# Performance work log

Hardware: AMD Instinct MI355X
Metric: run time of the kernel (lower is better)

Reference implementation:

```python
import jax, jax.numpy as jnp
import numpy as np

GAMMA = 1.0

C, K, D = 10000, 4, 2048  # classes, prototypes per class, feature dim


def setup_inputs() -> dict:
    key = jax.random.key(0)
    k1, k2 = jax.random.split(key)
    feature = jax.random.normal(k1, (D,), dtype=jnp.float32)
    all_prototypes = jax.random.normal(k2, (C, K, D), dtype=jnp.float32)
    label = 7
    return {"feature": feature, "label": label, "all_prototypes": all_prototypes}


def reference(feature, label, all_prototypes):
    # squared euclidean distance from feature to every prototype: [C, K]
    diff = all_prototypes - feature  # broadcast [C,K,D]
    d = jnp.sum(diff * diff, axis=-1)  # [C,K]
    logits = -GAMMA * d  # [C,K]
    # denominator: one = sum_{c,k} exp(-gamma * d_{c,k}); use stable logsumexp
    log_one = jax.nn.logsumexp(logits)
    # probability = sum_k -log(exp(logits[label,k]) / one)
    #             = sum_k (gamma * d[label,k] + log(one))
    lbl_logits = jax.lax.dynamic_index_in_dim(logits, label, axis=0, keepdims=False)  # [K]
    probability = jnp.sum(log_one - lbl_logits)
    return probability
```

## Files before the change

kernel.cpp:

```cpp
#include <hip/hip_runtime.h>

#define C_CLASSES 10000
#define K_PROTO   4
#define D_DIM     2048
#define ROWS      (C_CLASSES * K_PROTO)
#define D_VEC     (D_DIM / 4)

__global__ __launch_bounds__(256) void dist_kernel(const float4* __restrict__ proto,
                                                   const float4* __restrict__ feat,
                                                   float* __restrict__ d_row) {
    const int wave = threadIdx.x >> 6;
    const int lane = threadIdx.x & 63;
    const int row  = blockIdx.x * 4 + wave;
    const float4* p = proto + (size_t)row * D_VEC;

    float acc = 0.0f;
#pragma unroll
    for (int j = 0; j < 8; ++j) {
        const int idx = j * 64 + lane;
        const float4 pv = p[idx];
        const float4 fv = feat[idx];
        const float dx = pv.x - fv.x;
        const float dy = pv.y - fv.y;
        const float dz = pv.z - fv.z;
        const float dw = pv.w - fv.w;
        acc += dx * dx + dy * dy + dz * dz + dw * dw;
    }
#pragma unroll
    for (int off = 32; off > 0; off >>= 1)
        acc += __shfl_down(acc, off, 64);
    if (lane == 0) d_row[row] = acc;
}

__global__ __launch_bounds__(256) void finalize_kernel(const float* __restrict__ d_row,
                                                       const int* __restrict__ label,
                                                       float* __restrict__ out) {
    __shared__ float red[256];
    const int tid = threadIdx.x;

    float lmin = 3.402823466e38f;
    for (int i = tid; i < ROWS; i += 256)
        lmin = fminf(lmin, d_row[i]);
    red[tid] = lmin;
    __syncthreads();
    for (int s = 128; s > 0; s >>= 1) {
        if (tid < s) red[tid] = fminf(red[tid], red[tid + s]);
        __syncthreads();
    }
    const float dmin = red[0];
    __syncthreads();

    float lsum = 0.0f;
    for (int i = tid; i < ROWS; i += 256)
        lsum += expf(dmin - d_row[i]);
    red[tid] = lsum;
    __syncthreads();
    for (int s = 128; s > 0; s >>= 1) {
        if (tid < s) red[tid] += red[tid + s];
        __syncthreads();
    }

    if (tid == 0) {
        const float log_one = -dmin + logf(red[0]);
        const int lbl = label[0];
        float p = 0.0f;
#pragma unroll
        for (int k = 0; k < K_PROTO; ++k)
            p += log_one + d_row[lbl * K_PROTO + k];
        out[0] = p;
    }
}

extern "C" void kernel_launch(void* const* d_in, const int* in_sizes, int n_in,
                              void* d_out, int out_size, void* d_ws, size_t ws_size,
                              hipStream_t stream) {
    const float* feat  = (const float*)d_in[0];
    const int*   label = (const int*)d_in[1];
    const float* proto = (const float*)d_in[2];
    float* out   = (float*)d_out;
    float* d_row = (float*)d_ws;

    dist_kernel<<<ROWS / 4, 256, 0, stream>>>(
        (const float4*)proto, (const float4*)feat, d_row);
    finalize_kernel<<<1, 256, 0, stream>>>(d_row, label, out);
}
```

Before: 476.2 us.

## Process five rows per wave and fuse partial logsumexp into distance kernel

```diff
diff --git a/kernel.cpp b/kernel.cpp
--- a/kernel.cpp
+++ b/kernel.cpp
@@ -5,43 +5,73 @@
 #define D_DIM     2048
 #define ROWS      (C_CLASSES * K_PROTO)
 #define D_VEC     (D_DIM / 4)
+#define RPW       5
+#define NBLOCKS   2000
+#define NWAVES    (NBLOCKS * 4)
 
 __global__ __launch_bounds__(256) void dist_kernel(const float4* __restrict__ proto,
                                                    const float4* __restrict__ feat,
-                                                   float* __restrict__ d_row) {
-    const int wave = threadIdx.x >> 6;
+                                                   const int* __restrict__ label,
+                                                   float* __restrict__ wave_min,
+                                                   float* __restrict__ wave_sum,
+                                                   float* __restrict__ d_label) {
+    const int wave = (blockIdx.x << 2) | (threadIdx.x >> 6);
     const int lane = threadIdx.x & 63;
-    const int row  = blockIdx.x * 4 + wave;
-    const float4* p = proto + (size_t)row * D_VEC;
+    const int row0 = wave * RPW;
+    const int lbl  = label[0];
 
-    float acc = 0.0f;
+    float4 f[8];
 #pragma unroll
-    for (int j = 0; j < 8; ++j) {
-        const int idx = j * 64 + lane;
-        const float4 pv = p[idx];
-        const float4 fv = feat[idx];
-        const float dx = pv.x - fv.x;
-        const float dy = pv.y - fv.y;
-        const float dz = pv.z - fv.z;
-        const float dw = pv.w - fv.w;
-        acc += dx * dx + dy * dy + dz * dz + dw * dw;
+    for (int j = 0; j < 8; ++j) f[j] = feat[j * 64 + lane];
+
+    float d[RPW];
+#pragma unroll
+    for (int r = 0; r < RPW; ++r) {
+        const float4* p = proto + (size_t)(row0 + r) * D_VEC;
+        float acc = 0.0f;
+#pragma unroll
+        for (int j = 0; j < 8; ++j) {
+            const float4 pv = p[j * 64 + lane];
+            const float dx = pv.x - f[j].x;
+            const float dy = pv.y - f[j].y;
+            const float dz = pv.z - f[j].z;
+            const float dw = pv.w - f[j].w;
+            acc += dx * dx + dy * dy + dz * dz + dw * dw;
+        }
+#pragma unroll
+        for (int mask = 1; mask < 64; mask <<= 1)
+            acc += __shfl_xor(acc, mask, 64);
+        d[r] = acc;
     }
+
+    float mw = d[0];
 #pragma unroll
-    for (int off = 32; off > 0; off >>= 1)
-        acc += __shfl_down(acc, off, 64);
-    if (lane == 0) d_row[row] = acc;
+    for (int r = 1; r < RPW; ++r) mw = fminf(mw, d[r]);
+    float sw = 0.0f;
+#pragma unroll
+    for (int r = 0; r < RPW; ++r) sw += expf(mw - d[r]);
+
+    if (lane == 0) {
+        wave_min[wave] = mw;
+        wave_sum[wave] = sw;
+#pragma unroll
+        for (int r = 0; r < RPW; ++r) {
+            const int row = row0 + r;
+            if ((row >> 2) == lbl) d_label[row & 3] = d[r];
+        }
+    }
 }
 
-__global__ __launch_bounds__(256) void finalize_kernel(const float* __restrict__ d_row,
-                                                       const int* __restrict__ label,
+__global__ __launch_bounds__(256) void finalize_kernel(const float* __restrict__ wave_min,
+                                                       const float* __restrict__ wave_sum,
+                                                       const float* __restrict__ d_label,
                                                        float* __restrict__ out) {
     __shared__ float red[256];
     const int tid = threadIdx.x;
 
-    float lmin = 3.402823466e38f;
-    for (int i = tid; i < ROWS; i += 256)
-        lmin = fminf(lmin, d_row[i]);
-    red[tid] = lmin;
+    float m = 3.402823466e38f;
+    for (int i = tid; i < NWAVES; i += 256) m = fminf(m, wave_min[i]);
+    red[tid] = m;
     __syncthreads();
     for (int s = 128; s > 0; s >>= 1) {
         if (tid < s) red[tid] = fminf(red[tid], red[tid + s]);
@@ -50,10 +80,10 @@
     const float dmin = red[0];
     __syncthreads();
 
-    float lsum = 0.0f;
-    for (int i = tid; i < ROWS; i += 256)
-        lsum += expf(dmin - d_row[i]);
-    red[tid] = lsum;
+    float acc = 0.0f;
+    for (int i = tid; i < NWAVES; i += 256)
+        acc += wave_sum[i] * expf(dmin - wave_min[i]);
+    red[tid] = acc;
     __syncthreads();
     for (int s = 128; s > 0; s >>= 1) {
         if (tid < s) red[tid] += red[tid + s];
@@ -62,11 +92,9 @@
 
     if (tid == 0) {
         const float log_one = -dmin + logf(red[0]);
-        const int lbl = label[0];
         float p = 0.0f;
 #pragma unroll
-        for (int k = 0; k < K_PROTO; ++k)
-            p += log_one + d_row[lbl * K_PROTO + k];
+        for (int k = 0; k < K_PROTO; ++k) p += log_one + d_label[k];
         out[0] = p;
     }
 }
@@ -77,10 +105,14 @@
     const float* feat  = (const float*)d_in[0];
     const int*   label = (const int*)d_in[1];
     const float* proto = (const float*)d_in[2];
-    float* out   = (float*)d_out;
-    float* d_row = (float*)d_ws;
+    float* out = (float*)d_out;
 
-    dist_kernel<<<ROWS / 4, 256, 0, stream>>>(
-        (const float4*)proto, (const float4*)feat, d_row);
-    finalize_kernel<<<1, 256, 0, stream>>>(d_row, label, out);
+    float* wave_min = (float*)d_ws;
+    float* wave_sum = wave_min + NWAVES;
+    float* d_label  = wave_sum + NWAVES;
+
+    dist_kernel<<<NBLOCKS, 256, 0, stream>>>(
+        (const float4*)proto, (const float4*)feat, label,
+        wave_min, wave_sum, d_label);
+    finalize_kernel<<<1, 256, 0, stream>>>(wave_min, wave_sum, d_label, out);
 }
```

Measured after the change: 460.0 us. -3.4%, faster.
